# Optimization experiments

Measured on AMD Instinct MI355X. Metric: run time of the kernel, lower is better.

## Reference

```python
import jax, jax.numpy as jnp
import numpy as np

B, T, C = 2, 2048, 1024
N_HEAD, N_KV_HEAD, N_GLOBAL_HEAD = 16, 8, 8
HEAD_DIM = C // N_HEAD  # 64
Q_PER_KV = N_HEAD // N_KV_HEAD  # 2
N_GLOBAL_KV = N_GLOBAL_HEAD // Q_PER_KV  # 4
VE_GATE_CH = 32


def setup_inputs() -> dict:
    key = jax.random.key(0)
    ks = jax.random.split(key, 8)
    x = jax.random.normal(ks[0], (B, T, C), jnp.float32)
    ve = jax.random.normal(ks[1], (B, T, N_KV_HEAD * HEAD_DIM), jnp.float32)
    # rotary cos/sin: [T, 1, head_dim//2]
    half = HEAD_DIM // 2
    inv_freq = 1.0 / (10000.0 ** (np.arange(half, dtype=np.float32) / half))
    ang = np.arange(T, dtype=np.float32)[:, None] * inv_freq[None, :]
    cos = jnp.asarray(np.cos(ang))[:, None, :]
    sin = jnp.asarray(np.sin(ang))[:, None, :]
    s = 0.02
    Wq = jax.random.normal(ks[2], (C, N_HEAD * HEAD_DIM), jnp.float32) * s
    Wk = jax.random.normal(ks[3], (C, N_KV_HEAD * HEAD_DIM), jnp.float32) * s
    Wv = jax.random.normal(ks[4], (C, N_KV_HEAD * HEAD_DIM), jnp.float32) * s
    Wproj = jax.random.normal(ks[5], (C, C), jnp.float32) * s
    Wgate = jax.random.normal(ks[6], (VE_GATE_CH, N_KV_HEAD), jnp.float32) * s
    return {"x": x, "ve": ve, "cos": cos, "sin": sin, "Wq": Wq, "Wk": Wk,
            "Wv": Wv, "Wproj": Wproj, "Wgate": Wgate, "window": 512}


def _rope(x, cos, sin):
    # x: [B,T,H,D]; cos/sin: [T,1,D/2]
    d = x.shape[-1] // 2
    x1, x2 = x[..., :d], x[..., d:]
    return jnp.concatenate([x1 * cos + x2 * sin, -x1 * sin + x2 * cos], axis=-1)


def _rmsnorm(x):
    eps = jnp.finfo(x.dtype).eps
    return x * jax.lax.rsqrt(jnp.mean(x * x, axis=-1, keepdims=True) + eps)


def _attn(q, k, v, mask):
    # q,k,v: [B,T,H,D]; mask: [T,T] bool (True = allowed)
    scale = 1.0 / jnp.sqrt(jnp.asarray(q.shape[-1], q.dtype))
    scores = jnp.einsum('bqhd,bkhd->bhqk', q, k) * scale
    scores = jnp.where(mask[None, None], scores, jnp.finfo(scores.dtype).min)
    p = jax.nn.softmax(scores, axis=-1)
    return jnp.einsum('bhqk,bkhd->bqhd', p, v)


def reference(x, ve, cos, sin, Wq, Wk, Wv, Wproj, Wgate, window):
    q = (x @ Wq).reshape(B, T, N_HEAD, HEAD_DIM)
    k = (x @ Wk).reshape(B, T, N_KV_HEAD, HEAD_DIM)
    v = (x @ Wv).reshape(B, T, N_KV_HEAD, HEAD_DIM)
    # value-embedding gate
    gate = 2.0 * jax.nn.sigmoid(x[..., :VE_GATE_CH] @ Wgate)  # [B,T,n_kv]
    v = v + gate[..., None] * ve.reshape(B, T, N_KV_HEAD, HEAD_DIM)
    q, k = _rope(q, cos, sin), _rope(k, cos, sin)
    q, k = _rmsnorm(q), _rmsnorm(k)
    # split global / local heads
    qg, ql = q[:, :, :N_GLOBAL_HEAD], q[:, :, N_GLOBAL_HEAD:]
    kg, kl = k[:, :, :N_GLOBAL_KV], k[:, :, N_GLOBAL_KV:]
    vg, vl = v[:, :, :N_GLOBAL_KV], v[:, :, N_GLOBAL_KV:]
    # GQA: expand kv heads
    kg, vg = jnp.repeat(kg, Q_PER_KV, axis=2), jnp.repeat(vg, Q_PER_KV, axis=2)
    kl, vl = jnp.repeat(kl, Q_PER_KV, axis=2), jnp.repeat(vl, Q_PER_KV, axis=2)
    i = jnp.arange(T)[:, None]
    j = jnp.arange(T)[None, :]
    causal = j <= i
    local_mask = causal & (j >= i - window)  # flash window_size=(window, 0)
    yg = _attn(qg, kg, vg, causal)
    yl = _attn(ql, kl, vl, local_mask)
    y = jnp.concatenate([yg, yl], axis=2).reshape(B, T, C)
    return y @ Wproj
```

## Files before the change

### kernel.cpp

```cpp
#include <hip/hip_runtime.h>
#include <hip/hip_bf16.h>

#define BB 2
#define TT 2048
#define CC 1024
#define NH 16
#define NKV 8
#define HD 64

typedef __attribute__((ext_vector_type(8))) short short8;
typedef __attribute__((ext_vector_type(4))) float float4v;

__device__ __forceinline__ ushort f2bf(float f) {
    __hip_bfloat16 h = __float2bfloat16(f);
    union { __hip_bfloat16 h; ushort u; } v; v.h = h; return v.u;
}

__device__ __forceinline__ void gload16(const ushort* g, ushort* l) {
    __builtin_amdgcn_global_load_lds(
        (const __attribute__((address_space(1))) unsigned int*)g,
        (__attribute__((address_space(3))) unsigned int*)l, 16, 0, 0);
}

__global__ __launch_bounds__(256) void conv_kernel(
    const float* __restrict__ src, ushort* __restrict__ dst, int n)
{
    int i = (blockIdx.x * 256 + threadIdx.x) * 4;
    if (i + 3 < n) {
        float4 v = *(const float4*)&src[i];
        dst[i + 0] = f2bf(v.x);
        dst[i + 1] = f2bf(v.y);
        dst[i + 2] = f2bf(v.z);
        dst[i + 3] = f2bf(v.w);
    }
}

__global__ __launch_bounds__(256) void transpose_conv_kernel(
    const float* __restrict__ src, ushort* __restrict__ dst, int Kd, int Nd)
{
    __shared__ float tile[64][65];
    const int kt = blockIdx.x * 64, nt = blockIdx.y * 64;
    const int tid = threadIdx.x;
    {
        int r = tid >> 2, c = (tid & 3) * 16;
        #pragma unroll
        for (int i = 0; i < 4; i++) {
            float4 v = *(const float4*)&src[(size_t)(kt + r) * Nd + nt + c + i * 4];
            tile[r][c + i * 4 + 0] = v.x;
            tile[r][c + i * 4 + 1] = v.y;
            tile[r][c + i * 4 + 2] = v.z;
            tile[r][c + i * 4 + 3] = v.w;
        }
    }
    __syncthreads();
    {
        int n = tid >> 2, k = (tid & 3) * 16;
        #pragma unroll
        for (int i = 0; i < 2; i++) {
            ushort u[8];
            #pragma unroll
            for (int j = 0; j < 8; j++) u[j] = f2bf(tile[k + i * 8 + j][n]);
            *(uint4*)&dst[(size_t)(nt + n) * Kd + kt + k + i * 8] = *(uint4*)u;
        }
    }
}

__global__ __launch_bounds__(256) void gemm_bt_kernel(
    const ushort* __restrict__ A, const ushort* __restrict__ Bt,
    float* __restrict__ Cp, int M, int N, int K, int ldc)
{
    __shared__ ushort As[128][32];
    __shared__ ushort Bs[128][32];

    const int m0 = blockIdx.x * 128;
    const int n0 = blockIdx.y * 128;
    const int tid = threadIdx.x;
    const int lane = tid & 63;
    const int w = tid >> 6;
    const int lr = lane & 15, lc = lane >> 4;
    const int wm = (w >> 1) * 64, wn = (w & 1) * 64;

    float4v acc[4][4] = {};

    for (int k0 = 0; k0 < K; k0 += 32) {
        #pragma unroll
        for (int s = 0; s < 2; s++) {
            int rb = w * 32 + s * 16;
            gload16(&A [(size_t)(m0 + rb + (lane >> 2)) * K + k0 + (lane & 3) * 8], &As[rb][0]);
            gload16(&Bt[(size_t)(n0 + rb + (lane >> 2)) * K + k0 + (lane & 3) * 8], &Bs[rb][0]);
        }
        __syncthreads();

        short8 af[4], bf[4];
        #pragma unroll
        for (int t = 0; t < 4; t++) {
            af[t] = *(const short8*)&As[wm + t * 16 + lr][lc * 8];
            bf[t] = *(const short8*)&Bs[wn + t * 16 + lr][lc * 8];
        }
        #pragma unroll
        for (int rt = 0; rt < 4; rt++)
            #pragma unroll
            for (int ct = 0; ct < 4; ct++)
                acc[rt][ct] = __builtin_amdgcn_mfma_f32_16x16x32_bf16(af[rt], bf[ct], acc[rt][ct], 0, 0, 0);
        __syncthreads();
    }

    #pragma unroll
    for (int rt = 0; rt < 4; rt++)
        #pragma unroll
        for (int ct = 0; ct < 4; ct++)
            #pragma unroll
            for (int r = 0; r < 4; r++) {
                int row = m0 + wm + rt * 16 + lc * 4 + r;
                int col = n0 + wn + ct * 16 + lr;
                Cp[(size_t)row * ldc + col] = acc[rt][ct][r];
            }
}

__global__ __launch_bounds__(256) void qkv_post_kernel(
    const float* __restrict__ qkv, const float* __restrict__ x,
    const float* __restrict__ ve, const float* __restrict__ cosb,
    const float* __restrict__ sinb, const float* __restrict__ wgate,
    ushort* __restrict__ Qb, ushort* __restrict__ Kb, ushort* __restrict__ Vt)
{
    const int bt = blockIdx.x;
    const int b = bt >> 11, t = bt & 2047;
    const int tid = threadIdx.x;
    const int lane = tid & 63;
    const int w = tid >> 6;
    __shared__ float gateS[8];

    {
        int g = tid >> 5, i = tid & 31;
        float p = x[(size_t)bt * CC + i] * wgate[i * 8 + g];
        #pragma unroll
        for (int off = 16; off; off >>= 1) p += __shfl_down(p, off, 32);
        if (i == 0) gateS[g] = 2.f / (1.f + __expf(-p));
    }
    __syncthreads();

    const float c = cosb[t * 32 + (lane & 31)];
    const float s = sinb[t * 32 + (lane & 31)];
    for (int hh = w; hh < 24; hh += 4) {
        const float* z = &qkv[(size_t)bt * 2048 + hh * 64];
        float v = z[lane];
        float other = __shfl_xor(v, 32);
        float x1 = (lane < 32) ? v : other;
        float x2 = (lane < 32) ? other : v;
        float val = (lane < 32) ? (x1 * c + x2 * s) : (-x1 * s + x2 * c);
        float ss = val * val;
        #pragma unroll
        for (int off = 32; off; off >>= 1) ss += __shfl_xor(ss, off);
        float scale = rsqrtf(ss * (1.f / 64.f) + 1.1920929e-07f);
        ushort ob = f2bf(val * scale);
        if (hh < 16) Qb[(((size_t)b * NH + hh) * TT + t) * HD + lane] = ob;
        else         Kb[(((size_t)b * NKV + (hh - 16)) * TT + t) * HD + lane] = ob;
    }

    for (int e = tid; e < NKV * HD; e += 256) {
        int kh = e >> 6, d = e & 63;
        float v = qkv[(size_t)bt * 2048 + 1536 + e] + gateS[kh] * ve[(size_t)bt * 512 + e];
        Vt[(((size_t)b * NKV + kh) * HD + d) * TT + t] = f2bf(v);
    }
}

__global__ __launch_bounds__(256) void attn_kernel(
    const ushort* __restrict__ Qb, const ushort* __restrict__ Kb,
    const ushort* __restrict__ Vt, ushort* __restrict__ Yb,
    const int* __restrict__ winp)
{
    const int gid = blockIdx.x;
    int b, h, qw;
    if (gid < 1024) { qw = 63 - (gid >> 4); h = (gid >> 1) & 7; b = gid & 1; }
    else { int j = gid - 1024; qw = 63 - (j >> 4); h = 8 + ((j >> 1) & 7); b = j & 1; }

    const int q0 = qw * 32;
    const int kvh = h >> 1;
    const bool local = (h >= 8);
    int window = *winp;
    if (window < 0 || window > TT) window = TT;
    const int tid = threadIdx.x;
    const int w = tid >> 6;
    const int lane = tid & 63;
    const int lr = lane & 15, lc = lane >> 4;

    __shared__ ushort Ps[4][16][72];
    __shared__ float4v Ol[4][4][64];
    __shared__ float Ll[4][16];

    const ushort* qbase = &Qb[(((size_t)b * NH + h) * TT + q0) * HD];
    short8 qf[2][2];
    #pragma unroll
    for (int rt = 0; rt < 2; rt++)
        #pragma unroll
        for (int xh = 0; xh < 2; xh++)
            qf[rt][xh] = *(const short8*)&qbase[(size_t)(rt * 16 + lr) * HD + xh * 32 + lc * 8];

    float4v o[2][4] = {};
    float l_[2] = {0.f, 0.f};

    const ushort* Kbase = &Kb[((size_t)b * NKV + kvh) * TT * HD];
    const ushort* Vbase = &Vt[((size_t)b * NKV + kvh) * HD * TT];

    const int qlast = q0 + 31;
    int jstart = 0;
    if (local) { int js = q0 - window; if (js > 0) jstart = js & ~63; }
    const int j0first = jstart + w * 64;

    short8 kf[4][2];
    if (j0first <= qlast) {
        #pragma unroll
        for (int jt = 0; jt < 4; jt++) {
            const ushort* kp = &Kbase[(size_t)(j0first + jt * 16 + lr) * HD + lc * 8];
            kf[jt][0] = *(const short8*)kp;
            kf[jt][1] = *(const short8*)(kp + 32);
        }
    }

    for (int j0 = j0first; j0 <= qlast; j0 += 256) {
        short8 vf[4][2];
        #pragma unroll
        for (int ct = 0; ct < 4; ct++) {
            const ushort* vp = &Vbase[(size_t)(ct * 16 + lr) * TT + j0 + lc * 8];
            vf[ct][0] = *(const short8*)vp;
            vf[ct][1] = *(const short8*)(vp + 32);
        }
        short8 kn[4][2];
        const bool more = (j0 + 256 <= qlast);
        if (more) {
            #pragma unroll
            for (int jt = 0; jt < 4; jt++) {
                const ushort* kp = &Kbase[(size_t)(j0 + 256 + jt * 16 + lr) * HD + lc * 8];
                kn[jt][0] = *(const short8*)kp;
                kn[jt][1] = *(const short8*)(kp + 32);
            }
        }

        float4v st[2][4];
        #pragma unroll
        for (int jt = 0; jt < 4; jt++)
            #pragma unroll
            for (int rt = 0; rt < 2; rt++) {
                float4v z = {};
                z = __builtin_amdgcn_mfma_f32_16x16x32_bf16(kf[jt][0], qf[rt][0], z, 0, 0, 0);
                z = __builtin_amdgcn_mfma_f32_16x16x32_bf16(kf[jt][1], qf[rt][1], z, 0, 0, 0);
                st[rt][jt] = z;
            }

        const bool need_c = (j0 + 63 > q0);
        const bool need_w = local && (j0 < qlast - window);

        #pragma unroll
        for (int rt = 0; rt < 2; rt++) {
            const int qrow = q0 + rt * 16 + lr;
            float p[4][4];
            if (need_c || need_w) {
                #pragma unroll
                for (int jt = 0; jt < 4; jt++)
                    #pragma unroll
                    for (int r = 0; r < 4; r++) {
                        int key = j0 + jt * 16 + lc * 4 + r;
                        bool ok = (key <= qrow) && (!local || key >= qrow - window);
                        p[jt][r] = ok ? __expf(st[rt][jt][r] * 0.125f) : 0.f;
                    }
            } else {
                #pragma unroll
                for (int jt = 0; jt < 4; jt++)
                    #pragma unroll
                    for (int r = 0; r < 4; r++)
                        p[jt][r] = __expf(st[rt][jt][r] * 0.125f);
            }
            float s0 = (p[0][0] + p[0][1]) + (p[0][2] + p[0][3]);
            float s1 = (p[1][0] + p[1][1]) + (p[1][2] + p[1][3]);
            float s2 = (p[2][0] + p[2][1]) + (p[2][2] + p[2][3]);
            float s3 = (p[3][0] + p[3][1]) + (p[3][2] + p[3][3]);
            l_[rt] += (s0 + s1) + (s2 + s3);

            #pragma unroll
            for (int jt = 0; jt < 4; jt++) {
                ushort4 u;
                u.x = f2bf(p[jt][0]); u.y = f2bf(p[jt][1]);
                u.z = f2bf(p[jt][2]); u.w = f2bf(p[jt][3]);
                *(ushort4*)&Ps[w][lr][jt * 16 + lc * 4] = u;
            }
            short8 pb0 = *(const short8*)&Ps[w][lr][lc * 8];
            short8 pb1 = *(const short8*)&Ps[w][lr][32 + lc * 8];
            #pragma unroll
            for (int ct = 0; ct < 4; ct++) {
                o[rt][ct] = __builtin_amdgcn_mfma_f32_16x16x32_bf16(vf[ct][0], pb0, o[rt][ct], 0, 0, 0);
                o[rt][ct] = __builtin_amdgcn_mfma_f32_16x16x32_bf16(vf[ct][1], pb1, o[rt][ct], 0, 0, 0);
            }
        }

        if (more) {
            #pragma unroll
            for (int jt = 0; jt < 4; jt++) {
                kf[jt][0] = kn[jt][0];
                kf[jt][1] = kn[jt][1];
            }
        }
    }

    #pragma unroll
    for (int rt = 0; rt < 2; rt++) {
        l_[rt] += __shfl_xor(l_[rt], 16);
        l_[rt] += __shfl_xor(l_[rt], 32);
    }

    #pragma unroll
    for (int rt = 0; rt < 2; rt++) {
        #pragma unroll
        for (int ct = 0; ct < 4; ct++) Ol[w][ct][lane] = o[rt][ct];
        if (lc == 0) Ll[w][lr] = l_[rt];
        __syncthreads();

        {
            const int ct = w;
            float ltot = (Ll[0][lr] + Ll[1][lr]) + (Ll[2][lr] + Ll[3][lr]);
            float inv = 1.f / fmaxf(ltot, 1e-20f);
            float4v a0 = Ol[0][ct][lane], a1 = Ol[1][ct][lane];
            float4v a2 = Ol[2][ct][lane], a3 = Ol[3][ct][lane];
            int qrow = q0 + rt * 16 + lr;
            ushort4 u;
            u.x = f2bf(((a0[0] + a1[0]) + (a2[0] + a3[0])) * inv);
            u.y = f2bf(((a0[1] + a1[1]) + (a2[1] + a3[1])) * inv);
            u.z = f2bf(((a0[2] + a1[2]) + (a2[2] + a3[2])) * inv);
            u.w = f2bf(((a0[3] + a1[3]) + (a2[3] + a3[3])) * inv);
            *(ushort4*)&Yb[((size_t)b * TT + qrow) * CC + h * 64 + ct * 16 + lc * 4] = u;
        }
        if (rt == 0) __syncthreads();
    }
}

extern "C" void kernel_launch(void* const* d_in, const int* in_sizes, int n_in,
                              void* d_out, int out_size, void* d_ws, size_t ws_size,
                              hipStream_t stream) {
    (void)in_sizes; (void)n_in; (void)out_size; (void)ws_size;
    const float* x     = (const float*)d_in[0];
    const float* ve    = (const float*)d_in[1];
    const float* cosb  = (const float*)d_in[2];
    const float* sinb  = (const float*)d_in[3];
    const float* Wq    = (const float*)d_in[4];
    const float* Wk    = (const float*)d_in[5];
    const float* Wv    = (const float*)d_in[6];
    const float* Wproj = (const float*)d_in[7];
    const float* Wgate = (const float*)d_in[8];
    const int*   winp  = (const int*)d_in[9];
    float* out = (float*)d_out;

    char* ws = (char*)d_ws;
    float*  qkv   = (float*)ws;
    ushort* Yb    = (ushort*)ws;
    ushort* xb    = (ushort*)(ws + 33554432);
    ushort* WqkvT = (ushort*)(ws + 41943040);
    ushort* WpT   = (ushort*)(ws + 46137344);
    ushort* Qb    = (ushort*)(ws + 48234496);
    ushort* Kb    = (ushort*)(ws + 56623104);
    ushort* Vtb   = (ushort*)(ws + 60817408);

    dim3 blk(256);
    conv_kernel<<<dim3(4096), blk, 0, stream>>>(x, xb, BB * TT * CC);
    transpose_conv_kernel<<<dim3(16, 16), blk, 0, stream>>>(Wq, WqkvT, 1024, 1024);
    transpose_conv_kernel<<<dim3(16, 8), blk, 0, stream>>>(Wk, WqkvT + (size_t)1024 * 1024, 1024, 512);
    transpose_conv_kernel<<<dim3(16, 8), blk, 0, stream>>>(Wv, WqkvT + (size_t)1536 * 1024, 1024, 512);
    transpose_conv_kernel<<<dim3(16, 16), blk, 0, stream>>>(Wproj, WpT, 1024, 1024);
    gemm_bt_kernel<<<dim3(32, 16), blk, 0, stream>>>(xb, WqkvT, qkv, 4096, 2048, 1024, 2048);
    qkv_post_kernel<<<dim3(BB * TT), blk, 0, stream>>>(qkv, x, ve, cosb, sinb, Wgate, Qb, Kb, Vtb);
    attn_kernel<<<dim3(2048), blk, 0, stream>>>(Qb, Kb, Vtb, Yb, winp);
    gemm_bt_kernel<<<dim3(32, 8), blk, 0, stream>>>(Yb, WpT, out, 4096, 1024, 1024, 1024);
}
```

Baseline: 244.6 us.

## Merge prep kernels, coalesce V writes via transpose, smaller M-tile for proj GEMM

Folds the x conversion and the four weight transpose-conversions into one prep kernel, removing four launches. The qkv post kernel now writes V row-major, so its stores are coalesced instead of strided by T. A separate tiled kernel then transposes V for attention. The output projection GEMM is templated to a 64-row M tile, doubling its grid to 512 blocks for better CU occupancy. The cost is one extra launch and an extra pass over V.

```diff
diff --git a/kernel.cpp b/kernel.cpp
--- a/kernel.cpp
+++ b/kernel.cpp
@@ -22,34 +22,20 @@
         (__attribute__((address_space(3))) unsigned int*)l, 16, 0, 0);
 }
 
-__global__ __launch_bounds__(256) void conv_kernel(
-    const float* __restrict__ src, ushort* __restrict__ dst, int n)
-{
-    int i = (blockIdx.x * 256 + threadIdx.x) * 4;
-    if (i + 3 < n) {
-        float4 v = *(const float4*)&src[i];
-        dst[i + 0] = f2bf(v.x);
-        dst[i + 1] = f2bf(v.y);
-        dst[i + 2] = f2bf(v.z);
-        dst[i + 3] = f2bf(v.w);
-    }
-}
-
-__global__ __launch_bounds__(256) void transpose_conv_kernel(
-    const float* __restrict__ src, ushort* __restrict__ dst, int Kd, int Nd)
-{
-    __shared__ float tile[64][65];
-    const int kt = blockIdx.x * 64, nt = blockIdx.y * 64;
+__device__ __forceinline__ void transpose_tile(
+    const float* __restrict__ src, ushort* __restrict__ dst,
+    int Kd, int Nd, int kt, int nt, float* tile )
+{
     const int tid = threadIdx.x;
     {
         int r = tid >> 2, c = (tid & 3) * 16;
         #pragma unroll
         for (int i = 0; i < 4; i++) {
             float4 v = *(const float4*)&src[(size_t)(kt + r) * Nd + nt + c + i * 4];
-            tile[r][c + i * 4 + 0] = v.x;
-            tile[r][c + i * 4 + 1] = v.y;
-            tile[r][c + i * 4 + 2] = v.z;
-            tile[r][c + i * 4 + 3] = v.w;
+            tile[r * 65 + c + i * 4 + 0] = v.x;
+            tile[r * 65 + c + i * 4 + 1] = v.y;
+            tile[r * 65 + c + i * 4 + 2] = v.z;
+            tile[r * 65 + c + i * 4 + 3] = v.w;
         }
     }
     __syncthreads();
@@ -59,46 +45,85 @@
         for (int i = 0; i < 2; i++) {
             ushort u[8];
             #pragma unroll
-            for (int j = 0; j < 8; j++) u[j] = f2bf(tile[k + i * 8 + j][n]);
+            for (int j = 0; j < 8; j++) u[j] = f2bf(tile[(k + i * 8 + j) * 65 + n]);
             *(uint4*)&dst[(size_t)(nt + n) * Kd + kt + k + i * 8] = *(uint4*)u;
         }
     }
 }
 
+__global__ __launch_bounds__(256) void prep_kernel(
+    const float* __restrict__ x, ushort* __restrict__ xb,
+    const float* __restrict__ Wq, const float* __restrict__ Wk,
+    const float* __restrict__ Wv, const float* __restrict__ Wproj,
+    ushort* __restrict__ WqkvT, ushort* __restrict__ WpT)
+{
+    __shared__ float tile[64 * 65];
+    const int bid = blockIdx.x;
+    if (bid < 4096) {
+        int i = (bid * 256 + threadIdx.x) * 4;
+        float4 v = *(const float4*)&x[i];
+        xb[i + 0] = f2bf(v.x);
+        xb[i + 1] = f2bf(v.y);
+        xb[i + 2] = f2bf(v.z);
+        xb[i + 3] = f2bf(v.w);
+        return;
+    }
+    int t = bid - 4096;
+    if (t < 256) {
+        transpose_tile(Wq, WqkvT, 1024, 1024, (t >> 4) * 64, (t & 15) * 64, tile);
+    } else if (t < 384) {
+        t -= 256;
+        transpose_tile(Wk, WqkvT + (size_t)1024 * 1024, 1024, 512, (t >> 3) * 64, (t & 7) * 64, tile);
+    } else if (t < 512) {
+        t -= 384;
+        transpose_tile(Wv, WqkvT + (size_t)1536 * 1024, 1024, 512, (t >> 3) * 64, (t & 7) * 64, tile);
+    } else {
+        t -= 512;
+        transpose_tile(Wproj, WpT, 1024, 1024, (t >> 4) * 64, (t & 15) * 64, tile);
+    }
+}
+
+template<int BM>
 __global__ __launch_bounds__(256) void gemm_bt_kernel(
     const ushort* __restrict__ A, const ushort* __restrict__ Bt,
     float* __restrict__ Cp, int M, int N, int K, int ldc)
 {
-    __shared__ ushort As[128][32];
+    constexpr int RT = BM / 32;
+    __shared__ ushort As[BM][32];
     __shared__ ushort Bs[128][32];
 
-    const int m0 = blockIdx.x * 128;
+    const int m0 = blockIdx.x * BM;
     const int n0 = blockIdx.y * 128;
     const int tid = threadIdx.x;
     const int lane = tid & 63;
     const int w = tid >> 6;
     const int lr = lane & 15, lc = lane >> 4;
-    const int wm = (w >> 1) * 64, wn = (w & 1) * 64;
-
-    float4v acc[4][4] = {};
+    const int wm = (w >> 1) * (BM / 2), wn = (w & 1) * 64;
+
+    float4v acc[RT][4] = {};
 
     for (int k0 = 0; k0 < K; k0 += 32) {
+        #pragma unroll
+        for (int s = 0; s < BM / 64; s++) {
+            int rb = w * (BM / 4) + s * 16;
+            gload16(&A[(size_t)(m0 + rb + (lane >> 2)) * K + k0 + (lane & 3) * 8], &As[rb][0]);
+        }
         #pragma unroll
         for (int s = 0; s < 2; s++) {
             int rb = w * 32 + s * 16;
-            gload16(&A [(size_t)(m0 + rb + (lane >> 2)) * K + k0 + (lane & 3) * 8], &As[rb][0]);
             gload16(&Bt[(size_t)(n0 + rb + (lane >> 2)) * K + k0 + (lane & 3) * 8], &Bs[rb][0]);
         }
         __syncthreads();
 
-        short8 af[4], bf[4];
-        #pragma unroll
-        for (int t = 0; t < 4; t++) {
+        short8 af[RT], bf[4];
+        #pragma unroll
+        for (int t = 0; t < RT; t++)
             af[t] = *(const short8*)&As[wm + t * 16 + lr][lc * 8];
+        #pragma unroll
+        for (int t = 0; t < 4; t++)
             bf[t] = *(const short8*)&Bs[wn + t * 16 + lr][lc * 8];
-        }
-        #pragma unroll
-        for (int rt = 0; rt < 4; rt++)
+        #pragma unroll
+        for (int rt = 0; rt < RT; rt++)
             #pragma unroll
             for (int ct = 0; ct < 4; ct++)
                 acc[rt][ct] = __builtin_amdgcn_mfma_f32_16x16x32_bf16(af[rt], bf[ct], acc[rt][ct], 0, 0, 0);
@@ -106,7 +131,7 @@
     }
 
     #pragma unroll
-    for (int rt = 0; rt < 4; rt++)
+    for (int rt = 0; rt < RT; rt++)
         #pragma unroll
         for (int ct = 0; ct < 4; ct++)
             #pragma unroll
@@ -121,7 +146,7 @@
     const float* __restrict__ qkv, const float* __restrict__ x,
     const float* __restrict__ ve, const float* __restrict__ cosb,
     const float* __restrict__ sinb, const float* __restrict__ wgate,
-    ushort* __restrict__ Qb, ushort* __restrict__ Kb, ushort* __restrict__ Vt)
+    ushort* __restrict__ Qb, ushort* __restrict__ Kb, ushort* __restrict__ Vn)
 {
     const int bt = blockIdx.x;
     const int b = bt >> 11, t = bt & 2047;
@@ -160,7 +185,35 @@
     for (int e = tid; e < NKV * HD; e += 256) {
         int kh = e >> 6, d = e & 63;
         float v = qkv[(size_t)bt * 2048 + 1536 + e] + gateS[kh] * ve[(size_t)bt * 512 + e];
-        Vt[(((size_t)b * NKV + kh) * HD + d) * TT + t] = f2bf(v);
+        Vn[(((size_t)b * NKV + kh) * TT + t) * HD + d] = f2bf(v);
+    }
+}
+
+__global__ __launch_bounds__(256) void v_transpose_kernel(
+    const ushort* __restrict__ Vn, ushort* __restrict__ Vt)
+{
+    __shared__ ushort tile[64][72];
+    const int t0 = blockIdx.x * 64;
+    const int bh = blockIdx.y;
+    const ushort* src = &Vn[(size_t)bh * TT * HD + (size_t)t0 * HD];
+    ushort* dst = &Vt[(size_t)bh * HD * TT + t0];
+    const int tid = threadIdx.x;
+    {
+        int r = tid >> 2, c = (tid & 3) * 16;
+        #pragma unroll
+        for (int i = 0; i < 2; i++)
+            *(uint4*)&tile[r][c + i * 8] = *(const uint4*)&src[(size_t)r * HD + c + i * 8];
+    }
+    __syncthreads();
+    {
+        int d = tid >> 2, c = (tid & 3) * 16;
+        #pragma unroll
+        for (int i = 0; i < 2; i++) {
+            ushort u[8];
+            #pragma unroll
+            for (int j = 0; j < 8; j++) u[j] = tile[c + i * 8 + j][d];
+            *(uint4*)&dst[(size_t)d * TT + c + i * 8] = *(uint4*)u;
+        }
     }
 }
 
@@ -352,6 +405,7 @@
     float*  qkv   = (float*)ws;
     ushort* Yb    = (ushort*)ws;
     ushort* xb    = (ushort*)(ws + 33554432);
+    ushort* Vnb   = (ushort*)(ws + 33554432);
     ushort* WqkvT = (ushort*)(ws + 41943040);
     ushort* WpT   = (ushort*)(ws + 46137344);
     ushort* Qb    = (ushort*)(ws + 48234496);
@@ -359,13 +413,10 @@
     ushort* Vtb   = (ushort*)(ws + 60817408);
 
     dim3 blk(256);
-    conv_kernel<<<dim3(4096), blk, 0, stream>>>(x, xb, BB * TT * CC);
-    transpose_conv_kernel<<<dim3(16, 16), blk, 0, stream>>>(Wq, WqkvT, 1024, 1024);
-    transpose_conv_kernel<<<dim3(16, 8), blk, 0, stream>>>(Wk, WqkvT + (size_t)1024 * 1024, 1024, 512);
-    transpose_conv_kernel<<<dim3(16, 8), blk, 0, stream>>>(Wv, WqkvT + (size_t)1536 * 1024, 1024, 512);
-    transpose_conv_kernel<<<dim3(16, 16), blk, 0, stream>>>(Wproj, WpT, 1024, 1024);
-    gemm_bt_kernel<<<dim3(32, 16), blk, 0, stream>>>(xb, WqkvT, qkv, 4096, 2048, 1024, 2048);
-    qkv_post_kernel<<<dim3(BB * TT), blk, 0, stream>>>(qkv, x, ve, cosb, sinb, Wgate, Qb, Kb, Vtb);
+    prep_kernel<<<dim3(4864), blk, 0, stream>>>(x, xb, Wq, Wk, Wv, Wproj, WqkvT, WpT);
+    gemm_bt_kernel<128><<<dim3(32, 16), blk, 0, stream>>>(xb, WqkvT, qkv, 4096, 2048, 1024, 2048);
+    qkv_post_kernel<<<dim3(BB * TT), blk, 0, stream>>>(qkv, x, ve, cosb, sinb, Wgate, Qb, Kb, Vnb);
+    v_transpose_kernel<<<dim3(TT / 64, BB * NKV), blk, 0, stream>>>(Vnb, Vtb);
     attn_kernel<<<dim3(2048), blk, 0, stream>>>(Qb, Kb, Vtb, Yb, winp);
-    gemm_bt_kernel<<<dim3(32, 8), blk, 0, stream>>>(Yb, WpT, out, 4096, 1024, 1024, 1024);
-}
+    gemm_bt_kernel<64><<<dim3(64, 8), blk, 0, stream>>>(Yb, WpT, out, 4096, 1024, 1024, 1024);
+}
```

Result: faster. 222.2 us (-9.2%).
